# Kernel optimization log

Measured on AMD Instinct MI355X. Metric: run time of the kernel, lower is better.

The kernel has to match this reference:

```python
import jax, jax.numpy as jnp
import numpy as np

B, IN_CH, OUT_CH, STYLE_DIM, K, H, W = 16, 512, 512, 512, 3, 32, 32


def setup_inputs() -> dict:
    key = jax.random.key(0)
    k1, k2, k3, k4 = jax.random.split(key, 4)
    return {
        "x": jax.random.normal(k1, (B, IN_CH, H, W), dtype=jnp.float32),
        "style": jax.random.normal(k2, (B, STYLE_DIM), dtype=jnp.float32),
        "aff_weight": jax.random.normal(k3, (IN_CH, STYLE_DIM), dtype=jnp.float32),
        "aff_bias": jnp.zeros((IN_CH,), dtype=jnp.float32),
        "conv_weight": jax.random.normal(k4, (OUT_CH, IN_CH, K, K), dtype=jnp.float32),
    }


def reference(x, style, aff_weight, aff_bias, conv_weight):
    # EqualizedLinearAct with act='linear': y = style @ (W*scale)^T + bias
    style_dim = aff_weight.shape[1]
    aff_scale = 1.0 / np.sqrt(style_dim)  # gain=1.0
    s = style @ (aff_weight * aff_scale).T + aff_bias + 1.0  # [B, in]

    out_ch, in_ch, k, _ = conv_weight.shape
    w_scale = 1.0 / np.sqrt(in_ch * k * k)  # gain / sqrt(in*k*k)
    # per-sample modulated weights: [B, out, in, k, k]
    w = conv_weight[None, :, :, :, :] * s[:, None, :, None, None] * w_scale
    # demodulation
    d = jax.lax.rsqrt(jnp.sum(w * w, axis=(2, 3, 4), keepdims=True) + 1e-8)
    w = w * d

    # groups=B grouped conv == per-sample conv; up=1, flip_weight=True ->
    # plain cross-correlation (same as torch F.conv2d / lax conv default).
    def conv1(xi, wi):
        # xi: [in, H, W], wi: [out, in, k, k]
        return jax.lax.conv_general_dilated(
            xi[None], wi, window_strides=(1, 1), padding="SAME",
            dimension_numbers=("NCHW", "OIHW", "NCHW"))[0]

    return jax.vmap(conv1)(x, w)  # [B, out, H, W]
```

## Files before the change

kernel.cpp:

```cpp
#include <hip/hip_runtime.h>


#define BATCH   16
#define CIN     512
#define COUT    512
#define IMG     32
#define PAD_IMG 34

static constexpr float AFF_SCALE = 0.044194173824159216f;
static constexpr float W_SCALE   = 0.014731391274719739f;

typedef __bf16 bf16x8 __attribute__((ext_vector_type(8)));
typedef float  f32x4  __attribute__((ext_vector_type(4)));

__device__ inline unsigned short f2bf(float f) {
    union { float f; unsigned int u; } v; v.f = f;
    unsigned int u = v.u;
    unsigned int r = (u + 0x7FFFu + ((u >> 16) & 1u)) >> 16;
    return (unsigned short)r;
}

__device__ inline float waveReduceSum(float v) {
    #pragma unroll
    for (int off = 32; off > 0; off >>= 1) v += __shfl_xor(v, off, 64);
    return v;
}

__global__ void prep1(const float* __restrict__ cw,
                      const float* __restrict__ style,
                      const float* __restrict__ aw,
                      const float* __restrict__ ab,
                      unsigned short* __restrict__ w_t,
                      float* __restrict__ wsq,
                      float* __restrict__ s_out) {
    const int tid = threadIdx.x;
    if (blockIdx.x < 1024) {
        __shared__ float wl[2304];
        const float* src = cw + (size_t)blockIdx.x * 2304;
        for (int j = tid; j < 2304; j += 256) wl[j] = src[j];
        __syncthreads();
        const int idx = blockIdx.x * 256 + tid;
        const int base = tid * 9;
        float acc = 0.f;
        #pragma unroll
        for (int e = 0; e < 9; ++e) {
            float v = wl[base + e];
            acc += v * v;
            w_t[e * (COUT * CIN) + idx] = f2bf(v);
        }
        wsq[idx] = acc;
    } else {
        const int q = blockIdx.x - 1024;
        const int b = q >> 7;
        const int i = (q & 127) * 4 + (tid >> 6);
        const int lane = tid & 63;
        float sum = 0.f;
        #pragma unroll
        for (int k = 0; k < 512; k += 64)
            sum += style[b * 512 + k + lane] * aw[i * 512 + k + lane];
        sum = waveReduceSum(sum);
        if (lane == 0)
            s_out[b * 512 + i] = sum * AFF_SCALE + ab[i] + 1.0f;
    }
}

__global__ void prep2(const float* __restrict__ x,
                      const float* __restrict__ s_in,
                      const float* __restrict__ wsq,
                      unsigned short* __restrict__ xpad,
                      float* __restrict__ scl) {
    const int tid = threadIdx.x;
    if (blockIdx.x >= 4352) {
        const int q = blockIdx.x - 4352;
        const int b = q >> 7;
        const int o = (q & 127) * 4 + (tid >> 6);
        const int lane = tid & 63;
        float sum = 0.f;
        #pragma unroll
        for (int i = 0; i < 512; i += 64) {
            float sv = s_in[b * 512 + i + lane];
            sum += sv * sv * wsq[o * 512 + i + lane];
        }
        sum = waveReduceSum(sum);
        if (lane == 0)
            scl[b * 512 + o] = W_SCALE * rsqrtf(W_SCALE * W_SCALE * sum + 1e-8f);
        return;
    }
    const int c0   = blockIdx.x & 7;
    const int rest = blockIdx.x >> 3;
    const int hh   = rest % 34;
    const int b    = rest / 34;
    const int c0b  = c0 * 64;
    unsigned short* rowbase = xpad + (((size_t)b * PAD_IMG + hh) * PAD_IMG) * 512;

    if (hh == 0 || hh == PAD_IMG - 1) {
        for (int j = tid; j < 34 * 32; j += 256) {
            int ww = j >> 5, cp = (j & 31) * 2;
            *(unsigned int*)(rowbase + (size_t)ww * 512 + c0b + cp) = 0u;
        }
        return;
    }

    __shared__ float t[64][33];
    const int h = hh - 1;
    {
        const int wx = tid & 31;
        const int cb = (tid >> 5) * 8;
        const float* xb = x + (((size_t)b * 512 + c0b + cb) * IMG + h) * IMG + wx;
        #pragma unroll
        for (int j = 0; j < 8; ++j)
            t[cb + j][wx] = xb[(size_t)j * (IMG * IMG)] * s_in[b * 512 + c0b + cb + j];
    }
    __syncthreads();
    {
        const int p  = tid >> 3;
        const int cc = (tid & 7) * 8;
        unsigned short* dst = rowbase + (size_t)(p + 1) * 512 + c0b + cc;
        uint4 pk;
        pk.x = (unsigned)f2bf(t[cc + 0][p]) | ((unsigned)f2bf(t[cc + 1][p]) << 16);
        pk.y = (unsigned)f2bf(t[cc + 2][p]) | ((unsigned)f2bf(t[cc + 3][p]) << 16);
        pk.z = (unsigned)f2bf(t[cc + 4][p]) | ((unsigned)f2bf(t[cc + 5][p]) << 16);
        pk.w = (unsigned)f2bf(t[cc + 6][p]) | ((unsigned)f2bf(t[cc + 7][p]) << 16);
        *(uint4*)dst = pk;
    }
    if (tid < 64) {
        int ww = (tid >> 5) ? (PAD_IMG - 1) : 0;
        int cp = (tid & 31) * 2;
        *(unsigned int*)(rowbase + (size_t)ww * 512 + c0b + cp) = 0u;
    }
}


#define SYNC() do {                                                           \
    asm volatile("s_waitcnt lgkmcnt(0)" ::: "memory");                        \
    __builtin_amdgcn_s_barrier();                                             \
    __builtin_amdgcn_sched_barrier(0);                                        \
} while (0)

#define LOADSTEP(stp) do {                                                    \
    const int e_  = (stp) >> 3;                                               \
    const int kc_ = ((stp) & 7) << 6;                                         \
    const int kh_ = (e_ * 11) >> 5;                                           \
    const int kw_ = e_ - kh_ * 3;                                             \
    const unsigned short* Ab_ = wt + (size_t)e_ * (COUT * CIN)                \
                                   + (size_t)m0 * 512 + kc_;                  \
    const unsigned short* Bb_ = xpad + bImgBase                               \
                              + (size_t)((h0 + kh_) * PAD_IMG + kw_) * 512    \
                              + kc_;                                          \
    ra0 = *(const uint4*)(Ab_ + aOff0);                                       \
    ra1 = *(const uint4*)(Ab_ + aOff1);                                       \
    ra2 = *(const uint4*)(Ab_ + aOff2);                                       \
    ra3 = *(const uint4*)(Ab_ + aOff3);                                       \
    rb0 = *(const uint4*)(Bb_ + bOff0);                                       \
    rb1 = *(const uint4*)(Bb_ + bOff1);                                       \
    rb2 = *(const uint4*)(Bb_ + bOff2);                                       \
    rb3 = *(const uint4*)(Bb_ + bOff3);                                       \
} while (0)

__global__ __launch_bounds__(256, 2) void conv_mfma(
    const unsigned short* __restrict__ wt,
    const unsigned short* __restrict__ xpad,
    const float* __restrict__ scl,
    float* __restrict__ out)
{
    __shared__ __align__(16) unsigned short Alds[2][128 * 64];
    __shared__ __align__(16) unsigned short Blds[2][128 * 64];
    __shared__ float sclds[128];

    const int tid = threadIdx.x;
    const int id    = blockIdx.x;
    const int xcd   = id & 7;
    const int local = id >> 3;
    const int gp    = xcd * 16 + (local >> 2);
    const int m0  = (local & 3) * 128;
    const int h0  = (gp & 7) * 4;
    const int b   = gp >> 3;

    if (tid < 128) sclds[tid] = scl[b * 512 + m0 + tid];

    const int wid  = tid >> 6;
    const int lane = tid & 63;
    const int wm = wid & 1, wn = wid >> 1;

    const f32x4 vzero = {0.f, 0.f, 0.f, 0.f};
    f32x4 acc[4][4];
    #pragma unroll
    for (int i = 0; i < 4; ++i)
        #pragma unroll
        for (int j = 0; j < 4; ++j) acc[i][j] = vzero;

    int aOff0, aOff1, aOff2, aOff3;
    int bOff0, bOff1, bOff2, bOff3;
    int lOff0, lOff1, lOff2, lOff3;
    {
        int f, row, c, p;
        f = tid;             row = f >> 3; c = f & 7; p = c ^ (row & 7);
        aOff0 = row * 512 + c * 8;
        bOff0 = ((row >> 5) * PAD_IMG + (row & 31)) * 512 + c * 8;
        lOff0 = row * 64 + p * 8;
        f = 256 + tid;       row = f >> 3; c = f & 7; p = c ^ (row & 7);
        aOff1 = row * 512 + c * 8;
        bOff1 = ((row >> 5) * PAD_IMG + (row & 31)) * 512 + c * 8;
        lOff1 = row * 64 + p * 8;
        f = 512 + tid;       row = f >> 3; c = f & 7; p = c ^ (row & 7);
        aOff2 = row * 512 + c * 8;
        bOff2 = ((row >> 5) * PAD_IMG + (row & 31)) * 512 + c * 8;
        lOff2 = row * 64 + p * 8;
        f = 768 + tid;       row = f >> 3; c = f & 7; p = c ^ (row & 7);
        aOff3 = row * 512 + c * 8;
        bOff3 = ((row >> 5) * PAD_IMG + (row & 31)) * 512 + c * 8;
        lOff3 = row * 64 + p * 8;
    }

    const size_t bImgBase = (size_t)b * PAD_IMG * PAD_IMG * 512;

    uint4 ra0, ra1, ra2, ra3, rb0, rb1, rb2, rb3;

    LOADSTEP(0);

    const int rl   = lane & 15;
    const int kch  = lane >> 4;
    const int sw   = rl & 7;
    const int swz0 = (kch ^ sw) * 8;
    const int swz1 = ((kch + 4) ^ sw) * 8;
    const int arow = (wm * 64 + rl) * 64;
    const int brow = (wn * 64 + rl) * 64;

    for (int step = 0; step < 72; ++step) {
        const int buf = step & 1;
        *(uint4*)(&Alds[buf][lOff0]) = ra0;
        *(uint4*)(&Alds[buf][lOff1]) = ra1;
        *(uint4*)(&Alds[buf][lOff2]) = ra2;
        *(uint4*)(&Alds[buf][lOff3]) = ra3;
        *(uint4*)(&Blds[buf][lOff0]) = rb0;
        *(uint4*)(&Blds[buf][lOff1]) = rb1;
        *(uint4*)(&Blds[buf][lOff2]) = rb2;
        *(uint4*)(&Blds[buf][lOff3]) = rb3;
        const int nxt = step + 1 < 72 ? step + 1 : 71;
        LOADSTEP(nxt);
        SYNC();

        {
            bf16x8 af[4], bfr[4];
            #pragma unroll
            for (int mi = 0; mi < 4; ++mi)
                af[mi] = *(const bf16x8*)(&Alds[buf][arow + mi * (16 * 64) + swz0]);
            #pragma unroll
            for (int ni = 0; ni < 4; ++ni)
                bfr[ni] = *(const bf16x8*)(&Blds[buf][brow + ni * (16 * 64) + swz0]);
            __builtin_amdgcn_s_setprio(1);
            #pragma unroll
            for (int mi = 0; mi < 4; ++mi)
                #pragma unroll
                for (int ni = 0; ni < 4; ++ni)
                    acc[mi][ni] = __builtin_amdgcn_mfma_f32_16x16x32_bf16(
                        af[mi], bfr[ni], acc[mi][ni], 0, 0, 0);
            __builtin_amdgcn_s_setprio(0);
        }
        {
            bf16x8 af[4], bfr[4];
            #pragma unroll
            for (int mi = 0; mi < 4; ++mi)
                af[mi] = *(const bf16x8*)(&Alds[buf][arow + mi * (16 * 64) + swz1]);
            #pragma unroll
            for (int ni = 0; ni < 4; ++ni)
                bfr[ni] = *(const bf16x8*)(&Blds[buf][brow + ni * (16 * 64) + swz1]);
            __builtin_amdgcn_s_setprio(1);
            #pragma unroll
            for (int mi = 0; mi < 4; ++mi)
                #pragma unroll
                for (int ni = 0; ni < 4; ++ni)
                    acc[mi][ni] = __builtin_amdgcn_mfma_f32_16x16x32_bf16(
                        af[mi], bfr[ni], acc[mi][ni], 0, 0, 0);
            __builtin_amdgcn_s_setprio(0);
        }
    }

    const int colp = lane & 15;
    const int rowq = (lane >> 4) * 4;
    const int p0 = h0 * 32;
    #pragma unroll
    for (int mi = 0; mi < 4; ++mi) {
        #pragma unroll
        for (int ni = 0; ni < 4; ++ni) {
            const int p = p0 + wn * 64 + ni * 16 + colp;
            #pragma unroll
            for (int r2 = 0; r2 < 4; ++r2) {
                const int ol = wm * 64 + mi * 16 + rowq + r2;
                out[(((size_t)b * 512 + m0 + ol) << 10) + p] =
                    acc[mi][ni][r2] * sclds[ol];
            }
        }
    }
}

extern "C" void kernel_launch(void* const* d_in, const int* in_sizes, int n_in,
                              void* d_out, int out_size, void* d_ws, size_t ws_size,
                              hipStream_t stream) {
    const float* x     = (const float*)d_in[0];
    const float* style = (const float*)d_in[1];
    const float* aw    = (const float*)d_in[2];
    const float* ab    = (const float*)d_in[3];
    const float* cw    = (const float*)d_in[4];
    float* out = (float*)d_out;

    char* ws = (char*)d_ws;
    float* s_buf          = (float*)(ws);
    float* scl            = (float*)(ws + 32768);
    float* wsq            = (float*)(ws + 65536);
    unsigned short* w_t   = (unsigned short*)(ws + 1114112);
    unsigned short* x_pad = (unsigned short*)(ws + 5832704);

    prep1<<<dim3(3072), 256, 0, stream>>>(cw, style, aw, ab, w_t, wsq, s_buf);
    prep2<<<dim3(6400), 256, 0, stream>>>(x, s_buf, wsq, x_pad, scl);
    conv_mfma<<<dim3(512), 256, 0, stream>>>(w_t, x_pad, scl, out);
}
```

Baseline: 178.2 us.

## Enlarge conv MFMA tile to 256x128 per block with half the blocks

```diff
diff --git a/kernel.cpp b/kernel.cpp
--- a/kernel.cpp
+++ b/kernel.cpp
@@ -151,70 +151,103 @@
     ra1 = *(const uint4*)(Ab_ + aOff1);                                       \
     ra2 = *(const uint4*)(Ab_ + aOff2);                                       \
     ra3 = *(const uint4*)(Ab_ + aOff3);                                       \
+    ra4 = *(const uint4*)(Ab_ + aOff4);                                       \
+    ra5 = *(const uint4*)(Ab_ + aOff5);                                       \
+    ra6 = *(const uint4*)(Ab_ + aOff6);                                       \
+    ra7 = *(const uint4*)(Ab_ + aOff7);                                       \
     rb0 = *(const uint4*)(Bb_ + bOff0);                                       \
     rb1 = *(const uint4*)(Bb_ + bOff1);                                       \
     rb2 = *(const uint4*)(Bb_ + bOff2);                                       \
     rb3 = *(const uint4*)(Bb_ + bOff3);                                       \
 } while (0)
 
-__global__ __launch_bounds__(256, 2) void conv_mfma(
+#define COMMIT(bufidx) do {                                                   \
+    *(uint4*)(&Alds[bufidx][lA0]) = ra0;                                      \
+    *(uint4*)(&Alds[bufidx][lA1]) = ra1;                                      \
+    *(uint4*)(&Alds[bufidx][lA2]) = ra2;                                      \
+    *(uint4*)(&Alds[bufidx][lA3]) = ra3;                                      \
+    *(uint4*)(&Alds[bufidx][lA4]) = ra4;                                      \
+    *(uint4*)(&Alds[bufidx][lA5]) = ra5;                                      \
+    *(uint4*)(&Alds[bufidx][lA6]) = ra6;                                      \
+    *(uint4*)(&Alds[bufidx][lA7]) = ra7;                                      \
+    *(uint4*)(&Blds[bufidx][lB0]) = rb0;                                      \
+    *(uint4*)(&Blds[bufidx][lB1]) = rb1;                                      \
+    *(uint4*)(&Blds[bufidx][lB2]) = rb2;                                      \
+    *(uint4*)(&Blds[bufidx][lB3]) = rb3;                                      \
+} while (0)
+
+__global__ __launch_bounds__(256, 1) void conv_mfma(
     const unsigned short* __restrict__ wt,
     const unsigned short* __restrict__ xpad,
     const float* __restrict__ scl,
     float* __restrict__ out)
 {
-    __shared__ __align__(16) unsigned short Alds[2][128 * 64];
+    __shared__ __align__(16) unsigned short Alds[2][256 * 64];
     __shared__ __align__(16) unsigned short Blds[2][128 * 64];
-    __shared__ float sclds[128];
+    __shared__ float sclds[256];
 
     const int tid = threadIdx.x;
     const int id    = blockIdx.x;
     const int xcd   = id & 7;
     const int local = id >> 3;
-    const int gp    = xcd * 16 + (local >> 2);
-    const int m0  = (local & 3) * 128;
+    const int gp    = xcd * 16 + (local >> 1);
+    const int m0  = (local & 1) * 256;
     const int h0  = (gp & 7) * 4;
     const int b   = gp >> 3;
 
-    if (tid < 128) sclds[tid] = scl[b * 512 + m0 + tid];
+    sclds[tid] = scl[b * 512 + m0 + tid];
 
     const int wid  = tid >> 6;
     const int lane = tid & 63;
     const int wm = wid & 1, wn = wid >> 1;
 
     const f32x4 vzero = {0.f, 0.f, 0.f, 0.f};
-    f32x4 acc[4][4];
+    f32x4 acc[8][4];
     #pragma unroll
-    for (int i = 0; i < 4; ++i)
+    for (int i = 0; i < 8; ++i)
         #pragma unroll
         for (int j = 0; j < 4; ++j) acc[i][j] = vzero;
 
-    int aOff0, aOff1, aOff2, aOff3;
+    int aOff0, aOff1, aOff2, aOff3, aOff4, aOff5, aOff6, aOff7;
+    int lA0, lA1, lA2, lA3, lA4, lA5, lA6, lA7;
     int bOff0, bOff1, bOff2, bOff3;
-    int lOff0, lOff1, lOff2, lOff3;
+    int lB0, lB1, lB2, lB3;
     {
         int f, row, c, p;
-        f = tid;             row = f >> 3; c = f & 7; p = c ^ (row & 7);
-        aOff0 = row * 512 + c * 8;
+        f = 0 * 256 + tid; row = f >> 3; c = f & 7; p = c ^ (row & 7);
+        aOff0 = row * 512 + c * 8;  lA0 = row * 64 + p * 8;
+        f = 1 * 256 + tid; row = f >> 3; c = f & 7; p = c ^ (row & 7);
+        aOff1 = row * 512 + c * 8;  lA1 = row * 64 + p * 8;
+        f = 2 * 256 + tid; row = f >> 3; c = f & 7; p = c ^ (row & 7);
+        aOff2 = row * 512 + c * 8;  lA2 = row * 64 + p * 8;
+        f = 3 * 256 + tid; row = f >> 3; c = f & 7; p = c ^ (row & 7);
+        aOff3 = row * 512 + c * 8;  lA3 = row * 64 + p * 8;
+        f = 4 * 256 + tid; row = f >> 3; c = f & 7; p = c ^ (row & 7);
+        aOff4 = row * 512 + c * 8;  lA4 = row * 64 + p * 8;
+        f = 5 * 256 + tid; row = f >> 3; c = f & 7; p = c ^ (row & 7);
+        aOff5 = row * 512 + c * 8;  lA5 = row * 64 + p * 8;
+        f = 6 * 256 + tid; row = f >> 3; c = f & 7; p = c ^ (row & 7);
+        aOff6 = row * 512 + c * 8;  lA6 = row * 64 + p * 8;
+        f = 7 * 256 + tid; row = f >> 3; c = f & 7; p = c ^ (row & 7);
+        aOff7 = row * 512 + c * 8;  lA7 = row * 64 + p * 8;
+
+        f = 0 * 256 + tid; row = f >> 3; c = f & 7; p = c ^ (row & 7);
         bOff0 = ((row >> 5) * PAD_IMG + (row & 31)) * 512 + c * 8;
-        lOff0 = row * 64 + p * 8;
-        f = 256 + tid;       row = f >> 3; c = f & 7; p = c ^ (row & 7);
-        aOff1 = row * 512 + c * 8;
+        lB0 = row * 64 + p * 8;
+        f = 1 * 256 + tid; row = f >> 3; c = f & 7; p = c ^ (row & 7);
         bOff1 = ((row >> 5) * PAD_IMG + (row & 31)) * 512 + c * 8;
-        lOff1 = row * 64 + p * 8;
-        f = 512 + tid;       row = f >> 3; c = f & 7; p = c ^ (row & 7);
-        aOff2 = row * 512 + c * 8;
+        lB1 = row * 64 + p * 8;
+        f = 2 * 256 + tid; row = f >> 3; c = f & 7; p = c ^ (row & 7);
         bOff2 = ((row >> 5) * PAD_IMG + (row & 31)) * 512 + c * 8;
-        lOff2 = row * 64 + p * 8;
-        f = 768 + tid;       row = f >> 3; c = f & 7; p = c ^ (row & 7);
-        aOff3 = row * 512 + c * 8;
+        lB2 = row * 64 + p * 8;
+        f = 3 * 256 + tid; row = f >> 3; c = f & 7; p = c ^ (row & 7);
         bOff3 = ((row >> 5) * PAD_IMG + (row & 31)) * 512 + c * 8;
-        lOff3 = row * 64 + p * 8;
+        lB3 = row * 64 + p * 8;
     }
 
     const size_t bImgBase = (size_t)b * PAD_IMG * PAD_IMG * 512;
 
-    uint4 ra0, ra1, ra2, ra3, rb0, rb1, rb2, rb3;
+    uint4 ra0, ra1, ra2, ra3, ra4, ra5, ra6, ra7, rb0, rb1, rb2, rb3;
 
     LOADSTEP(0);
 
@@ -223,70 +256,57 @@
     const int sw   = rl & 7;
     const int swz0 = (kch ^ sw) * 8;
     const int swz1 = ((kch + 4) ^ sw) * 8;
-    const int arow = (wm * 64 + rl) * 64;
+    const int arow = (wm * 128 + rl) * 64;
     const int brow = (wn * 64 + rl) * 64;
 
     for (int step = 0; step < 72; ++step) {
         const int buf = step & 1;
-        *(uint4*)(&Alds[buf][lOff0]) = ra0;
-        *(uint4*)(&Alds[buf][lOff1]) = ra1;
-        *(uint4*)(&Alds[buf][lOff2]) = ra2;
-        *(uint4*)(&Alds[buf][lOff3]) = ra3;
-        *(uint4*)(&Blds[buf][lOff0]) = rb0;
-        *(uint4*)(&Blds[buf][lOff1]) = rb1;
-        *(uint4*)(&Blds[buf][lOff2]) = rb2;
-        *(uint4*)(&Blds[buf][lOff3]) = rb3;
+        COMMIT(buf);
         const int nxt = step + 1 < 72 ? step + 1 : 71;
         LOADSTEP(nxt);
         SYNC();
 
-        {
-            bf16x8 af[4], bfr[4];
-            #pragma unroll
-            for (int mi = 0; mi < 4; ++mi)
-                af[mi] = *(const bf16x8*)(&Alds[buf][arow + mi * (16 * 64) + swz0]);
+        bf16x8 a0[8], b0[4], a1[8], b1[4];
+        #pragma unroll
+        for (int mi = 0; mi < 8; ++mi)
+            a0[mi] = *(const bf16x8*)(&Alds[buf][arow + mi * (16 * 64) + swz0]);
+        #pragma unroll
+        for (int ni = 0; ni < 4; ++ni)
+            b0[ni] = *(const bf16x8*)(&Blds[buf][brow + ni * (16 * 64) + swz0]);
+        #pragma unroll
+        for (int mi = 0; mi < 8; ++mi)
+            a1[mi] = *(const bf16x8*)(&Alds[buf][arow + mi * (16 * 64) + swz1]);
+        #pragma unroll
+        for (int ni = 0; ni < 4; ++ni)
+            b1[ni] = *(const bf16x8*)(&Blds[buf][brow + ni * (16 * 64) + swz1]);
+
+        __builtin_amdgcn_s_setprio(1);
+        #pragma unroll
+        for (int mi = 0; mi < 8; ++mi)
             #pragma unroll
             for (int ni = 0; ni < 4; ++ni)
-                bfr[ni] = *(const bf16x8*)(&Blds[buf][brow + ni * (16 * 64) + swz0]);
-            __builtin_amdgcn_s_setprio(1);
-            #pragma unroll
-            for (int mi = 0; mi < 4; ++mi)
-                #pragma unroll
-                for (int ni = 0; ni < 4; ++ni)
-                    acc[mi][ni] = __builtin_amdgcn_mfma_f32_16x16x32_bf16(
-                        af[mi], bfr[ni], acc[mi][ni], 0, 0, 0);
-            __builtin_amdgcn_s_setprio(0);
-        }
-        {
-            bf16x8 af[4], bfr[4];
-            #pragma unroll
-            for (int mi = 0; mi < 4; ++mi)
-                af[mi] = *(const bf16x8*)(&Alds[buf][arow + mi * (16 * 64) + swz1]);
+                acc[mi][ni] = __builtin_amdgcn_mfma_f32_16x16x32_bf16(
+                    a0[mi], b0[ni], acc[mi][ni], 0, 0, 0);
+        #pragma unroll
+        for (int mi = 0; mi < 8; ++mi)
             #pragma unroll
             for (int ni = 0; ni < 4; ++ni)
-                bfr[ni] = *(const bf16x8*)(&Blds[buf][brow + ni * (16 * 64) + swz1]);
-            __builtin_amdgcn_s_setprio(1);
-            #pragma unroll
-            for (int mi = 0; mi < 4; ++mi)
-                #pragma unroll
-                for (int ni = 0; ni < 4; ++ni)
-                    acc[mi][ni] = __builtin_amdgcn_mfma_f32_16x16x32_bf16(
-                        af[mi], bfr[ni], acc[mi][ni], 0, 0, 0);
-            __builtin_amdgcn_s_setprio(0);
-        }
+                acc[mi][ni] = __builtin_amdgcn_mfma_f32_16x16x32_bf16(
+                    a1[mi], b1[ni], acc[mi][ni], 0, 0, 0);
+        __builtin_amdgcn_s_setprio(0);
     }
 
     const int colp = lane & 15;
     const int rowq = (lane >> 4) * 4;
     const int p0 = h0 * 32;
     #pragma unroll
-    for (int mi = 0; mi < 4; ++mi) {
+    for (int mi = 0; mi < 8; ++mi) {
         #pragma unroll
         for (int ni = 0; ni < 4; ++ni) {
             const int p = p0 + wn * 64 + ni * 16 + colp;
             #pragma unroll
             for (int r2 = 0; r2 < 4; ++r2) {
-                const int ol = wm * 64 + mi * 16 + rowq + r2;
+                const int ol = wm * 128 + mi * 16 + rowq + r2;
                 out[(((size_t)b * 512 + m0 + ol) << 10) + p] =
                     acc[mi][ni][r2] * sclds[ol];
             }
@@ -313,5 +333,5 @@
 
     prep1<<<dim3(3072), 256, 0, stream>>>(cw, style, aw, ab, w_t, wsq, s_buf);
     prep2<<<dim3(6400), 256, 0, stream>>>(x, s_buf, wsq, x_pad, scl);
-    conv_mfma<<<dim3(512), 256, 0, stream>>>(w_t, x_pad, scl, out);
-}
+    conv_mfma<<<dim3(256), 256, 0, stream>>>(w_t, x_pad, scl, out);
+}
```

Measured after the change: 216.6 us. 21.5% more time.

## Enlarge conv tile to 128x256 with 8 waves and intra-block split-K reduction

Applied to the files above, without the earlier changes.

```diff
diff --git a/kernel.cpp b/kernel.cpp
--- a/kernel.cpp
+++ b/kernel.cpp
@@ -149,146 +149,149 @@
                               + kc_;                                          \
     ra0 = *(const uint4*)(Ab_ + aOff0);                                       \
     ra1 = *(const uint4*)(Ab_ + aOff1);                                       \
-    ra2 = *(const uint4*)(Ab_ + aOff2);                                       \
-    ra3 = *(const uint4*)(Ab_ + aOff3);                                       \
     rb0 = *(const uint4*)(Bb_ + bOff0);                                       \
     rb1 = *(const uint4*)(Bb_ + bOff1);                                       \
     rb2 = *(const uint4*)(Bb_ + bOff2);                                       \
     rb3 = *(const uint4*)(Bb_ + bOff3);                                       \
 } while (0)
 
-__global__ __launch_bounds__(256, 2) void conv_mfma(
+#define COMMIT(Albuf, Blbuf) do {                                             \
+    *(uint4*)((Albuf) + lA0) = ra0;                                           \
+    *(uint4*)((Albuf) + lA1) = ra1;                                           \
+    *(uint4*)((Blbuf) + lB0) = rb0;                                           \
+    *(uint4*)((Blbuf) + lB1) = rb1;                                           \
+    *(uint4*)((Blbuf) + lB2) = rb2;                                           \
+    *(uint4*)((Blbuf) + lB3) = rb3;                                           \
+} while (0)
+
+__global__ __launch_bounds__(512, 2) void conv_mfma(
     const unsigned short* __restrict__ wt,
     const unsigned short* __restrict__ xpad,
     const float* __restrict__ scl,
     float* __restrict__ out)
 {
-    __shared__ __align__(16) unsigned short Alds[2][128 * 64];
-    __shared__ __align__(16) unsigned short Blds[2][128 * 64];
+    __shared__ __align__(16) unsigned char smem[98304];
+    unsigned short* Alds0 = (unsigned short*)(smem);
+    unsigned short* Alds1 = (unsigned short*)(smem + 16384);
+    unsigned short* Blds0 = (unsigned short*)(smem + 32768);
+    unsigned short* Blds1 = (unsigned short*)(smem + 65536);
     __shared__ float sclds[128];
 
     const int tid = threadIdx.x;
     const int id    = blockIdx.x;
     const int xcd   = id & 7;
     const int local = id >> 3;
-    const int gp    = xcd * 16 + (local >> 2);
+    const int gp    = xcd * 8 + (local >> 2);
     const int m0  = (local & 3) * 128;
-    const int h0  = (gp & 7) * 4;
-    const int b   = gp >> 3;
+    const int b   = gp >> 2;
+    const int h0  = (gp & 3) * 8;
 
     if (tid < 128) sclds[tid] = scl[b * 512 + m0 + tid];
 
     const int wid  = tid >> 6;
     const int lane = tid & 63;
-    const int wm = wid & 1, wn = wid >> 1;
+    const int wm = (wid >> 1) & 1;
+    const int wn = wid & 1;
+    const int kg = wid >> 2;
 
     const f32x4 vzero = {0.f, 0.f, 0.f, 0.f};
-    f32x4 acc[4][4];
+    f32x4 acc[4][8];
     #pragma unroll
     for (int i = 0; i < 4; ++i)
         #pragma unroll
-        for (int j = 0; j < 4; ++j) acc[i][j] = vzero;
-
-    int aOff0, aOff1, aOff2, aOff3;
-    int bOff0, bOff1, bOff2, bOff3;
-    int lOff0, lOff1, lOff2, lOff3;
+        for (int j = 0; j < 8; ++j) acc[i][j] = vzero;
+
+    int aOff0, aOff1, lA0, lA1;
+    int bOff0, bOff1, bOff2, bOff3, lB0, lB1, lB2, lB3;
     {
         int f, row, c, p;
-        f = tid;             row = f >> 3; c = f & 7; p = c ^ (row & 7);
-        aOff0 = row * 512 + c * 8;
+        f = tid;              row = f >> 3; c = f & 7; p = c ^ (row & 7);
+        aOff0 = row * 512 + c * 8;  lA0 = row * 64 + p * 8;
+        f = 512 + tid;        row = f >> 3; c = f & 7; p = c ^ (row & 7);
+        aOff1 = row * 512 + c * 8;  lA1 = row * 64 + p * 8;
+
+        f = tid;              row = f >> 3; c = f & 7; p = c ^ (row & 7);
         bOff0 = ((row >> 5) * PAD_IMG + (row & 31)) * 512 + c * 8;
-        lOff0 = row * 64 + p * 8;
-        f = 256 + tid;       row = f >> 3; c = f & 7; p = c ^ (row & 7);
-        aOff1 = row * 512 + c * 8;
+        lB0 = row * 64 + p * 8;
+        f = 512 + tid;        row = f >> 3; c = f & 7; p = c ^ (row & 7);
         bOff1 = ((row >> 5) * PAD_IMG + (row & 31)) * 512 + c * 8;
-        lOff1 = row * 64 + p * 8;
-        f = 512 + tid;       row = f >> 3; c = f & 7; p = c ^ (row & 7);
-        aOff2 = row * 512 + c * 8;
+        lB1 = row * 64 + p * 8;
+        f = 1024 + tid;       row = f >> 3; c = f & 7; p = c ^ (row & 7);
         bOff2 = ((row >> 5) * PAD_IMG + (row & 31)) * 512 + c * 8;
-        lOff2 = row * 64 + p * 8;
-        f = 768 + tid;       row = f >> 3; c = f & 7; p = c ^ (row & 7);
-        aOff3 = row * 512 + c * 8;
+        lB2 = row * 64 + p * 8;
+        f = 1536 + tid;       row = f >> 3; c = f & 7; p = c ^ (row & 7);
         bOff3 = ((row >> 5) * PAD_IMG + (row & 31)) * 512 + c * 8;
-        lOff3 = row * 64 + p * 8;
+        lB3 = row * 64 + p * 8;
     }
 
     const size_t bImgBase = (size_t)b * PAD_IMG * PAD_IMG * 512;
 
-    uint4 ra0, ra1, ra2, ra3, rb0, rb1, rb2, rb3;
+    uint4 ra0, ra1, rb0, rb1, rb2, rb3;
 
     LOADSTEP(0);
 
     const int rl   = lane & 15;
     const int kch  = lane >> 4;
-    const int sw   = rl & 7;
-    const int swz0 = (kch ^ sw) * 8;
-    const int swz1 = ((kch + 4) ^ sw) * 8;
+    const int swz  = ((kg * 4 + kch) ^ (rl & 7)) * 8;
     const int arow = (wm * 64 + rl) * 64;
-    const int brow = (wn * 64 + rl) * 64;
+    const int brow = (wn * 128 + rl) * 64;
 
     for (int step = 0; step < 72; ++step) {
-        const int buf = step & 1;
-        *(uint4*)(&Alds[buf][lOff0]) = ra0;
-        *(uint4*)(&Alds[buf][lOff1]) = ra1;
-        *(uint4*)(&Alds[buf][lOff2]) = ra2;
-        *(uint4*)(&Alds[buf][lOff3]) = ra3;
-        *(uint4*)(&Blds[buf][lOff0]) = rb0;
-        *(uint4*)(&Blds[buf][lOff1]) = rb1;
-        *(uint4*)(&Blds[buf][lOff2]) = rb2;
-        *(uint4*)(&Blds[buf][lOff3]) = rb3;
+        unsigned short* Ab_lds = (step & 1) ? Alds1 : Alds0;
+        unsigned short* Bb_lds = (step & 1) ? Blds1 : Blds0;
+        COMMIT(Ab_lds, Bb_lds);
         const int nxt = step + 1 < 72 ? step + 1 : 71;
         LOADSTEP(nxt);
         SYNC();
 
-        {
-            bf16x8 af[4], bfr[4];
+        bf16x8 af[4], bfr[8];
+        #pragma unroll
+        for (int mi = 0; mi < 4; ++mi)
+            af[mi] = *(const bf16x8*)(Ab_lds + arow + mi * (16 * 64) + swz);
+        #pragma unroll
+        for (int ni = 0; ni < 8; ++ni)
+            bfr[ni] = *(const bf16x8*)(Bb_lds + brow + ni * (16 * 64) + swz);
+
+        __builtin_amdgcn_s_setprio(1);
+        #pragma unroll
+        for (int mi = 0; mi < 4; ++mi)
             #pragma unroll
-            for (int mi = 0; mi < 4; ++mi)
-                af[mi] = *(const bf16x8*)(&Alds[buf][arow + mi * (16 * 64) + swz0]);
-            #pragma unroll
-            for (int ni = 0; ni < 4; ++ni)
-                bfr[ni] = *(const bf16x8*)(&Blds[buf][brow + ni * (16 * 64) + swz0]);
-            __builtin_amdgcn_s_setprio(1);
+            for (int ni = 0; ni < 8; ++ni)
+                acc[mi][ni] = __builtin_amdgcn_mfma_f32_16x16x32_bf16(
+                    af[mi], bfr[ni], acc[mi][ni], 0, 0, 0);
+        __builtin_amdgcn_s_setprio(0);
+    }
+
+    const int colp = lane & 15;
+    const int rowq = (lane >> 4) * 4;
+    float* ep = (float*)smem;
+    float* reg = ep + wn * 8192;
+    for (int wmr = 0; wmr < 2; ++wmr) {
+        __syncthreads();
+        if (wm == wmr && kg == 1) {
             #pragma unroll
             for (int mi = 0; mi < 4; ++mi)
                 #pragma unroll
-                for (int ni = 0; ni < 4; ++ni)
-                    acc[mi][ni] = __builtin_amdgcn_mfma_f32_16x16x32_bf16(
-                        af[mi], bfr[ni], acc[mi][ni], 0, 0, 0);
-            __builtin_amdgcn_s_setprio(0);
-        }
-        {
-            bf16x8 af[4], bfr[4];
+                for (int ni = 0; ni < 8; ++ni)
+                    *(f32x4*)(reg + ((mi * 8 + ni) * 64 + lane) * 4) =
+                        acc[mi][ni];
+        }
+        __syncthreads();
+        if (wm == wmr && kg == 0) {
             #pragma unroll
-            for (int mi = 0; mi < 4; ++mi)
-                af[mi] = *(const bf16x8*)(&Alds[buf][arow + mi * (16 * 64) + swz1]);
-            #pragma unroll
-            for (int ni = 0; ni < 4; ++ni)
-                bfr[ni] = *(const bf16x8*)(&Blds[buf][brow + ni * (16 * 64) + swz1]);
-            __builtin_amdgcn_s_setprio(1);
-            #pragma unroll
-            for (int mi = 0; mi < 4; ++mi)
+            for (int mi = 0; mi < 4; ++mi) {
                 #pragma unroll
-                for (int ni = 0; ni < 4; ++ni)
-                    acc[mi][ni] = __builtin_amdgcn_mfma_f32_16x16x32_bf16(
-                        af[mi], bfr[ni], acc[mi][ni], 0, 0, 0);
-            __builtin_amdgcn_s_setprio(0);
-        }
-    }
-
-    const int colp = lane & 15;
-    const int rowq = (lane >> 4) * 4;
-    const int p0 = h0 * 32;
-    #pragma unroll
-    for (int mi = 0; mi < 4; ++mi) {
-        #pragma unroll
-        for (int ni = 0; ni < 4; ++ni) {
-            const int p = p0 + wn * 64 + ni * 16 + colp;
-            #pragma unroll
-            for (int r2 = 0; r2 < 4; ++r2) {
-                const int ol = wm * 64 + mi * 16 + rowq + r2;
-                out[(((size_t)b * 512 + m0 + ol) << 10) + p] =
-                    acc[mi][ni][r2] * sclds[ol];
+                for (int ni = 0; ni < 8; ++ni) {
+                    const f32x4 o =
+                        *(const f32x4*)(reg + ((mi * 8 + ni) * 64 + lane) * 4);
+                    const int p = h0 * 32 + wn * 128 + ni * 16 + colp;
+                    #pragma unroll
+                    for (int r2 = 0; r2 < 4; ++r2) {
+                        const int ol = wm * 64 + mi * 16 + rowq + r2;
+                        out[(((size_t)b * 512 + m0 + ol) << 10) + p] =
+                            (acc[mi][ni][r2] + o[r2]) * sclds[ol];
+                    }
+                }
             }
         }
     }
@@ -313,5 +316,5 @@
 
     prep1<<<dim3(3072), 256, 0, stream>>>(cw, style, aw, ab, w_t, wsq, s_buf);
     prep2<<<dim3(6400), 256, 0, stream>>>(x, s_buf, wsq, x_pad, scl);
-    conv_mfma<<<dim3(512), 256, 0, stream>>>(w_t, x_pad, scl, out);
-}
+    conv_mfma<<<dim3(256), 512, 0, stream>>>(w_t, x_pad, scl, out);
+}
```

Result: faster. 168.5 us (-5.4%).

## Split K across wave pairs with single LDS buffer and LDS reduction epilogue

Applied to the files above, without the earlier changes.

```diff
diff --git a/kernel.cpp b/kernel.cpp
--- a/kernel.cpp
+++ b/kernel.cpp
@@ -157,14 +157,26 @@
     rb3 = *(const uint4*)(Bb_ + bOff3);                                       \
 } while (0)
 
+#define COMMIT() do {                                                         \
+    *(uint4*)(Alds + lOff0) = ra0;                                            \
+    *(uint4*)(Alds + lOff1) = ra1;                                            \
+    *(uint4*)(Alds + lOff2) = ra2;                                            \
+    *(uint4*)(Alds + lOff3) = ra3;                                            \
+    *(uint4*)(Blds + lOff0) = rb0;                                            \
+    *(uint4*)(Blds + lOff1) = rb1;                                            \
+    *(uint4*)(Blds + lOff2) = rb2;                                            \
+    *(uint4*)(Blds + lOff3) = rb3;                                            \
+} while (0)
+
 __global__ __launch_bounds__(256, 2) void conv_mfma(
     const unsigned short* __restrict__ wt,
     const unsigned short* __restrict__ xpad,
     const float* __restrict__ scl,
     float* __restrict__ out)
 {
-    __shared__ __align__(16) unsigned short Alds[2][128 * 64];
-    __shared__ __align__(16) unsigned short Blds[2][128 * 64];
+    __shared__ __align__(16) unsigned char smem[32768];
+    unsigned short* Alds = (unsigned short*)smem;
+    unsigned short* Blds = (unsigned short*)(smem + 16384);
     __shared__ float sclds[128];
 
     const int tid = threadIdx.x;
@@ -180,14 +192,15 @@
 
     const int wid  = tid >> 6;
     const int lane = tid & 63;
-    const int wm = wid & 1, wn = wid >> 1;
+    const int wm = wid & 1;
+    const int kg = wid >> 1;
 
     const f32x4 vzero = {0.f, 0.f, 0.f, 0.f};
-    f32x4 acc[4][4];
+    f32x4 acc[4][8];
     #pragma unroll
     for (int i = 0; i < 4; ++i)
         #pragma unroll
-        for (int j = 0; j < 4; ++j) acc[i][j] = vzero;
+        for (int j = 0; j < 8; ++j) acc[i][j] = vzero;
 
     int aOff0, aOff1, aOff2, aOff3;
     int bOff0, bOff1, bOff2, bOff3;
@@ -220,75 +233,65 @@
 
     const int rl   = lane & 15;
     const int kch  = lane >> 4;
-    const int sw   = rl & 7;
-    const int swz0 = (kch ^ sw) * 8;
-    const int swz1 = ((kch + 4) ^ sw) * 8;
+    const int swz  = ((kg * 4 + kch) ^ (rl & 7)) * 8;
     const int arow = (wm * 64 + rl) * 64;
-    const int brow = (wn * 64 + rl) * 64;
+    const int brow = rl * 64;
 
     for (int step = 0; step < 72; ++step) {
-        const int buf = step & 1;
-        *(uint4*)(&Alds[buf][lOff0]) = ra0;
-        *(uint4*)(&Alds[buf][lOff1]) = ra1;
-        *(uint4*)(&Alds[buf][lOff2]) = ra2;
-        *(uint4*)(&Alds[buf][lOff3]) = ra3;
-        *(uint4*)(&Blds[buf][lOff0]) = rb0;
-        *(uint4*)(&Blds[buf][lOff1]) = rb1;
-        *(uint4*)(&Blds[buf][lOff2]) = rb2;
-        *(uint4*)(&Blds[buf][lOff3]) = rb3;
+        COMMIT();
         const int nxt = step + 1 < 72 ? step + 1 : 71;
         LOADSTEP(nxt);
         SYNC();
 
-        {
-            bf16x8 af[4], bfr[4];
+        bf16x8 af[4], bfr[8];
+        #pragma unroll
+        for (int mi = 0; mi < 4; ++mi)
+            af[mi] = *(const bf16x8*)(Alds + arow + mi * (16 * 64) + swz);
+        #pragma unroll
+        for (int ni = 0; ni < 8; ++ni)
+            bfr[ni] = *(const bf16x8*)(Blds + brow + ni * (16 * 64) + swz);
+
+        __builtin_amdgcn_s_setprio(1);
+        #pragma unroll
+        for (int mi = 0; mi < 4; ++mi)
             #pragma unroll
-            for (int mi = 0; mi < 4; ++mi)
-                af[mi] = *(const bf16x8*)(&Alds[buf][arow + mi * (16 * 64) + swz0]);
-            #pragma unroll
-            for (int ni = 0; ni < 4; ++ni)
-                bfr[ni] = *(const bf16x8*)(&Blds[buf][brow + ni * (16 * 64) + swz0]);
-            __builtin_amdgcn_s_setprio(1);
+            for (int ni = 0; ni < 8; ++ni)
+                acc[mi][ni] = __builtin_amdgcn_mfma_f32_16x16x32_bf16(
+                    af[mi], bfr[ni], acc[mi][ni], 0, 0, 0);
+        __builtin_amdgcn_s_setprio(0);
+
+        SYNC();
+    }
+
+    const int colp = lane & 15;
+    const int rowq = (lane >> 4) * 4;
+    float* ep = (float*)smem;
+    for (int wmr = 0; wmr < 2; ++wmr) {
+        __syncthreads();
+        if (wm == wmr && kg == 1) {
             #pragma unroll
             for (int mi = 0; mi < 4; ++mi)
                 #pragma unroll
-                for (int ni = 0; ni < 4; ++ni)
-                    acc[mi][ni] = __builtin_amdgcn_mfma_f32_16x16x32_bf16(
-                        af[mi], bfr[ni], acc[mi][ni], 0, 0, 0);
-            __builtin_amdgcn_s_setprio(0);
-        }
-        {
-            bf16x8 af[4], bfr[4];
+                for (int ni = 0; ni < 8; ++ni)
+                    *(f32x4*)(ep + ((mi * 8 + ni) * 64 + lane) * 4) =
+                        acc[mi][ni];
+        }
+        __syncthreads();
+        if (wm == wmr && kg == 0) {
             #pragma unroll
-            for (int mi = 0; mi < 4; ++mi)
-                af[mi] = *(const bf16x8*)(&Alds[buf][arow + mi * (16 * 64) + swz1]);
-            #pragma unroll
-            for (int ni = 0; ni < 4; ++ni)
-                bfr[ni] = *(const bf16x8*)(&Blds[buf][brow + ni * (16 * 64) + swz1]);
-            __builtin_amdgcn_s_setprio(1);
-            #pragma unroll
-            for (int mi = 0; mi < 4; ++mi)
+            for (int mi = 0; mi < 4; ++mi) {
                 #pragma unroll
-                for (int ni = 0; ni < 4; ++ni)
-                    acc[mi][ni] = __builtin_amdgcn_mfma_f32_16x16x32_bf16(
-                        af[mi], bfr[ni], acc[mi][ni], 0, 0, 0);
-            __builtin_amdgcn_s_setprio(0);
-        }
-    }
-
-    const int colp = lane & 15;
-    const int rowq = (lane >> 4) * 4;
-    const int p0 = h0 * 32;
-    #pragma unroll
-    for (int mi = 0; mi < 4; ++mi) {
-        #pragma unroll
-        for (int ni = 0; ni < 4; ++ni) {
-            const int p = p0 + wn * 64 + ni * 16 + colp;
-            #pragma unroll
-            for (int r2 = 0; r2 < 4; ++r2) {
-                const int ol = wm * 64 + mi * 16 + rowq + r2;
-                out[(((size_t)b * 512 + m0 + ol) << 10) + p] =
-                    acc[mi][ni][r2] * sclds[ol];
+                for (int ni = 0; ni < 8; ++ni) {
+                    const f32x4 o =
+                        *(const f32x4*)(ep + ((mi * 8 + ni) * 64 + lane) * 4);
+                    const int p = h0 * 32 + ni * 16 + colp;
+                    #pragma unroll
+                    for (int r2 = 0; r2 < 4; ++r2) {
+                        const int ol = wmr * 64 + mi * 16 + rowq + r2;
+                        out[(((size_t)b * 512 + m0 + ol) << 10) + p] =
+                            (acc[mi][ni][r2] + o[r2]) * sclds[ol];
+                    }
+                }
             }
         }
     }
```

Result: no change. 175.7 us (-1.4%).
